# Kernel tuning notes

Measured on AMD Instinct MI355X. Metric: run time of the kernel, lower is better.

## Reference

```python
import jax, jax.numpy as jnp
import numpy as np


def _conv_nchw(x, w, strides):
    # F.conv2d with padding=0 -> VALID, NCHW / OIHW layout
    return jax.lax.conv_general_dilated(
        x, w, window_strides=tuple(strides), padding="VALID",
        dimension_numbers=("NCHW", "OIHW", "NCHW"))


def setup_inputs() -> dict:
    key = jax.random.key(0)
    kx, kw, kb = jax.random.split(key, 3)
    # scale so values span the full int8 range and all 8 bit-planes are active
    x = jax.random.normal(kx, (64, 64, 56, 56), dtype=jnp.float32) * 60.0
    weight = jax.random.normal(kw, (128, 64, 3, 3), dtype=jnp.float32) * 0.05
    bias = jax.random.normal(kb, (128,), dtype=jnp.float32)
    return {"x": x, "weight": weight, "bias": bias}


def reference(x, weight, bias):
    strides = (1, 1)
    # clamp to int8 range and cast (torch.clamp + .type(torch.int8))
    xi = jnp.clip(x, -128, 127).astype(jnp.int8)
    y = jnp.zeros((), dtype=weight.dtype)
    for i in range(8):
        # arithmetic shift on signed int8, matching torch semantics
        bit = ((xi >> i) & 1).astype(weight.dtype)
        yi = jnp.clip(_conv_nchw(bit, weight, strides), -1024, 1023)
        scale = jnp.asarray(-128.0 if i == 7 else float(2 ** i), dtype=weight.dtype)
        y = y + yi * scale
    y = y + bias.reshape(1, -1, 1, 1)
    return y
```

## Files before the change

### kernel.cpp

```cpp
#include <hip/hip_runtime.h>
#include <stdint.h>

typedef unsigned short u16;
typedef __attribute__((ext_vector_type(8))) __bf16 bf16x8;
typedef __attribute__((ext_vector_type(4))) float f32x4;

#define N_IMG 64
#define C_IN  64
#define HW_IN 3136
#define W_IN  56
#define C_OUT 128
#define OH    54
#define OW    54
#define SPI   2916
#define KTOT  576
#define M_TOTAL (N_IMG*SPI)

typedef __attribute__((address_space(3))) unsigned int lds_uint;
typedef __attribute__((address_space(1))) unsigned int gbl_uint;

__device__ __forceinline__ void load16_to_lds(const u16* g, u16* l) {
  __builtin_amdgcn_global_load_lds((const gbl_uint*)g, (lds_uint*)l, 16, 0, 0);
}

__device__ inline u16 f32_bf16_rne(float f) {
  unsigned u = __float_as_uint(f);
  u = (u + 0x7FFFu + ((u >> 16) & 1u)) >> 16;
  return (u16)u;
}

__global__ void convert_w(const float* __restrict__ w, u16* __restrict__ wtT) {
  int o = blockIdx.x * 256 + threadIdx.x;
  if (o >= C_OUT * KTOT) return;
  int co = o / KTOT;
  int k  = o - co * KTOT;
  int t  = k >> 6;
  int ci = k & 63;
  wtT[o] = f32_bf16_rne(w[co * KTOT + ci * 9 + t]);
}

__global__ __launch_bounds__(256) void convert_x(const float* __restrict__ x,
                                                 u16* __restrict__ xt) {
  __shared__ u16 tile[64][66];
  int n  = blockIdx.y;
  int s0 = blockIdx.x * 64;
  int tx = threadIdx.x, ty = threadIdx.y;
  const float* xp = x + (size_t)n * C_IN * HW_IN;
  #pragma unroll
  for (int i = ty; i < 64; i += 4) {
    float v = xp[i * HW_IN + s0 + tx];
    v = fminf(fmaxf(v, -128.f), 127.f);
    int iv = (int)v;
    tile[i][tx] = f32_bf16_rne((float)iv);
  }
  __syncthreads();
  u16* op = xt + (size_t)n * HW_IN * C_IN;
  #pragma unroll
  for (int i = ty; i < 64; i += 4) {
    op[(size_t)(s0 + i) * C_IN + tx] = tile[tx][i];
  }
}

__global__ __launch_bounds__(256) void conv_gemm(
    const u16* __restrict__ xt, const u16* __restrict__ wtT,
    const float* __restrict__ bias, float* __restrict__ y)
{
  __shared__ u16 sP[128 * 64];
  __shared__ u16 sW[128 * 64];

  int tid  = threadIdx.x;
  int wv   = tid >> 6;
  int lane = tid & 63;
  int ln   = lane & 15;
  int q    = lane >> 4;
  int wy   = wv >> 1;
  int wx   = wv & 1;

  int blk_sp0 = blockIdx.x * 128;

  int r8 = lane >> 3;
  int cg = lane & 7;
  int scol = (cg ^ r8) * 8;

  int pix_off[4], wt_off[4];
  #pragma unroll
  for (int j = 0; j < 4; j++) {
    int srow = wv * 32 + j * 8 + r8;
    int p   = blk_sp0 + srow;
    int img = p / SPI;  int rem = p - img * SPI;
    int oh  = rem / OW; int ow  = rem - oh * OW;
    pix_off[j] = (img * HW_IN + oh * W_IN + ow) * C_IN + scol;
    wt_off[j]  = srow * KTOT + scol;
  }

  f32x4 acc[4][4];
  #pragma unroll
  for (int mt = 0; mt < 4; mt++)
    #pragma unroll
    for (int nt = 0; nt < 4; nt++)
      acc[mt][nt] = (f32x4){0.f, 0.f, 0.f, 0.f};

  int wrow[4], prow[4];
  #pragma unroll
  for (int i = 0; i < 4; i++) {
    wrow[i] = (wy * 64 + i * 16 + ln) * 64;
    prow[i] = (wx * 64 + i * 16 + ln) * 64;
  }
  int l7 = ln & 7;

  #pragma unroll
  for (int kc = 0; kc < 9; kc++) {
    int kh = kc / 3, kw = kc - kh * 3;
    int xoff = (kh * W_IN + kw) * C_IN;

    __syncthreads();
    #pragma unroll
    for (int j = 0; j < 4; j++)
      load16_to_lds(xt + pix_off[j] + xoff, sP + (wv * 32 + j * 8) * 64);
    #pragma unroll
    for (int j = 0; j < 4; j++)
      load16_to_lds(wtT + wt_off[j] + kc * 64, sW + (wv * 32 + j * 8) * 64);
    __syncthreads();

    #pragma unroll
    for (int s = 0; s < 2; s++) {
      int pg = ((s * 4 + q) ^ l7) * 8;
      bf16x8 wf[4], pf[4];
      #pragma unroll
      for (int mt = 0; mt < 4; mt++)
        wf[mt] = *(const bf16x8*)(sW + wrow[mt] + pg);
      #pragma unroll
      for (int nt = 0; nt < 4; nt++)
        pf[nt] = *(const bf16x8*)(sP + prow[nt] + pg);
      #pragma unroll
      for (int mt = 0; mt < 4; mt++)
        #pragma unroll
        for (int nt = 0; nt < 4; nt++)
          acc[mt][nt] = __builtin_amdgcn_mfma_f32_16x16x32_bf16(
              wf[mt], pf[nt], acc[mt][nt], 0, 0, 0);
    }
  }

  #pragma unroll
  for (int nt = 0; nt < 4; nt++) {
    int p   = blk_sp0 + wx * 64 + nt * 16 + ln;
    int img = p / SPI;  int rem = p - img * SPI;
    int oh  = rem / OW; int ow  = rem - oh * OW;
    int obase = img * C_OUT * SPI + oh * OW + ow;
    #pragma unroll
    for (int mt = 0; mt < 4; mt++) {
      int co0 = wy * 64 + mt * 16 + q * 4;
      #pragma unroll
      for (int r = 0; r < 4; r++) {
        int co = co0 + r;
        y[obase + co * SPI] = acc[mt][nt][r] + bias[co];
      }
    }
  }
}

extern "C" void kernel_launch(void* const* d_in, const int* in_sizes, int n_in,
                              void* d_out, int out_size, void* d_ws, size_t ws_size,
                              hipStream_t stream) {
  const float* x    = (const float*)d_in[0];
  const float* w    = (const float*)d_in[1];
  const float* bias = (const float*)d_in[2];
  float* y = (float*)d_out;

  u16* wtT = (u16*)d_ws;
  u16* xt  = (u16*)((char*)d_ws + (size_t)C_OUT * KTOT * sizeof(u16));

  hipLaunchKernelGGL(convert_w, dim3((C_OUT * KTOT + 255) / 256), dim3(256), 0, stream,
                     w, wtT);
  hipLaunchKernelGGL(convert_x, dim3(HW_IN / 64, N_IMG), dim3(64, 4), 0, stream,
                     x, xt);
  hipLaunchKernelGGL(conv_gemm, dim3(M_TOTAL / 128), dim3(256), 0, stream,
                     xt, wtT, bias, y);
}
```

Baseline: 187.1 us.

## Double-buffer conv GEMM LDS tiles and fuse vectorized input/weight conversion

The conv GEMM now keeps two LDS buffers for the pixel and weight tiles. It prefetches the next 3x3 tap's slice while MFMAs run on the current one, which removes one barrier per tap and hides global-load latency. The separate weight and input conversion kernels are merged into one launch: an extra grid row handles the weights, and the input transpose uses 16-byte float4 loads and 8-wide u16 stores. The trade-off is that doubling LDS per block to 64 KB may lower how many blocks fit on each CU.

```diff
diff --git a/kernel.cpp b/kernel.cpp
--- a/kernel.cpp
+++ b/kernel.cpp
@@ -4,6 +4,8 @@
 typedef unsigned short u16;
 typedef __attribute__((ext_vector_type(8))) __bf16 bf16x8;
 typedef __attribute__((ext_vector_type(4))) float f32x4;
+typedef __attribute__((ext_vector_type(4))) u16 u16x4;
+typedef __attribute__((ext_vector_type(8))) u16 u16x8;
 
 #define N_IMG 64
 #define C_IN  64
@@ -29,35 +31,54 @@
   return (u16)u;
 }
 
-__global__ void convert_w(const float* __restrict__ w, u16* __restrict__ wtT) {
-  int o = blockIdx.x * 256 + threadIdx.x;
-  if (o >= C_OUT * KTOT) return;
-  int co = o / KTOT;
-  int k  = o - co * KTOT;
-  int t  = k >> 6;
-  int ci = k & 63;
-  wtT[o] = f32_bf16_rne(w[co * KTOT + ci * 9 + t]);
-}
-
-__global__ __launch_bounds__(256) void convert_x(const float* __restrict__ x,
-                                                 u16* __restrict__ xt) {
-  __shared__ u16 tile[64][66];
+__global__ __launch_bounds__(256) void convert_xw(
+    const float* __restrict__ x, const float* __restrict__ w,
+    u16* __restrict__ xt, u16* __restrict__ wtT)
+{
+  if (blockIdx.y == N_IMG) {
+    int o = blockIdx.x * 256 + threadIdx.x;
+    for (; o < C_OUT * KTOT; o += 49 * 256) {
+      int co = o / KTOT;
+      int k  = o - co * KTOT;
+      int t  = k >> 6;
+      int ci = k & 63;
+      wtT[o] = f32_bf16_rne(w[co * KTOT + ci * 9 + t]);
+    }
+    return;
+  }
+
+  __shared__ u16 tile[64][68];
   int n  = blockIdx.y;
   int s0 = blockIdx.x * 64;
-  int tx = threadIdx.x, ty = threadIdx.y;
-  const float* xp = x + (size_t)n * C_IN * HW_IN;
-  #pragma unroll
-  for (int i = ty; i < 64; i += 4) {
-    float v = xp[i * HW_IN + s0 + tx];
-    v = fminf(fmaxf(v, -128.f), 127.f);
-    int iv = (int)v;
-    tile[i][tx] = f32_bf16_rne((float)iv);
+  int t  = threadIdx.x;
+
+  int r = t >> 2;
+  int q = t & 3;
+  const float* xp = x + (size_t)n * C_IN * HW_IN + (size_t)r * HW_IN + s0 + q * 16;
+  #pragma unroll
+  for (int j = 0; j < 4; j++) {
+    f32x4 v = *(const f32x4*)(xp + 4 * j);
+    u16x4 o4;
+    #pragma unroll
+    for (int e = 0; e < 4; e++) {
+      float f = fminf(fmaxf(v[e], -128.f), 127.f);
+      int iv = (int)f;
+      o4[e] = f32_bf16_rne((float)iv);
+    }
+    *(u16x4*)&tile[r][q * 16 + 4 * j] = o4;
   }
   __syncthreads();
-  u16* op = xt + (size_t)n * HW_IN * C_IN;
-  #pragma unroll
-  for (int i = ty; i < 64; i += 4) {
-    op[(size_t)(s0 + i) * C_IN + tx] = tile[tx][i];
+
+  u16* op = xt + ((size_t)n * HW_IN + s0) * C_IN;
+  int g = t & 7;
+  int m = t >> 3;
+  #pragma unroll
+  for (int k2 = 0; k2 < 2; k2++) {
+    int sp = m * 2 + k2;
+    u16x8 o8;
+    #pragma unroll
+    for (int c = 0; c < 8; c++) o8[c] = tile[g * 8 + c][sp];
+    *(u16x8*)&op[(size_t)sp * C_IN + g * 8] = o8;
   }
 }
 
@@ -65,8 +86,8 @@
     const u16* __restrict__ xt, const u16* __restrict__ wtT,
     const float* __restrict__ bias, float* __restrict__ y)
 {
-  __shared__ u16 sP[128 * 64];
-  __shared__ u16 sW[128 * 64];
+  __shared__ u16 sP[2][128 * 64];
+  __shared__ u16 sW[2][128 * 64];
 
   int tid  = threadIdx.x;
   int wv   = tid >> 6;
@@ -107,20 +128,32 @@
     prow[i] = (wx * 64 + i * 16 + ln) * 64;
   }
   int l7 = ln & 7;
+  int lbase = (wv * 32) * 64;
+
+  #pragma unroll
+  for (int j = 0; j < 4; j++)
+    load16_to_lds(xt + pix_off[j], &sP[0][lbase + j * 8 * 64]);
+  #pragma unroll
+  for (int j = 0; j < 4; j++)
+    load16_to_lds(wtT + wt_off[j], &sW[0][lbase + j * 8 * 64]);
 
   #pragma unroll
   for (int kc = 0; kc < 9; kc++) {
-    int kh = kc / 3, kw = kc - kh * 3;
-    int xoff = (kh * W_IN + kw) * C_IN;
+    const int cur = kc & 1, nxt = cur ^ 1;
 
     __syncthreads();
-    #pragma unroll
-    for (int j = 0; j < 4; j++)
-      load16_to_lds(xt + pix_off[j] + xoff, sP + (wv * 32 + j * 8) * 64);
-    #pragma unroll
-    for (int j = 0; j < 4; j++)
-      load16_to_lds(wtT + wt_off[j] + kc * 64, sW + (wv * 32 + j * 8) * 64);
-    __syncthreads();
+
+    if (kc < 8) {
+      int kn = kc + 1;
+      int kh = kn / 3, kw = kn - kh * 3;
+      int xoff = (kh * W_IN + kw) * C_IN;
+      #pragma unroll
+      for (int j = 0; j < 4; j++)
+        load16_to_lds(xt + pix_off[j] + xoff, &sP[nxt][lbase + j * 8 * 64]);
+      #pragma unroll
+      for (int j = 0; j < 4; j++)
+        load16_to_lds(wtT + wt_off[j] + kn * 64, &sW[nxt][lbase + j * 8 * 64]);
+    }
 
     #pragma unroll
     for (int s = 0; s < 2; s++) {
@@ -128,10 +161,10 @@
       bf16x8 wf[4], pf[4];
       #pragma unroll
       for (int mt = 0; mt < 4; mt++)
-        wf[mt] = *(const bf16x8*)(sW + wrow[mt] + pg);
+        wf[mt] = *(const bf16x8*)(&sW[cur][0] + wrow[mt] + pg);
       #pragma unroll
       for (int nt = 0; nt < 4; nt++)
-        pf[nt] = *(const bf16x8*)(sP + prow[nt] + pg);
+        pf[nt] = *(const bf16x8*)(&sP[cur][0] + prow[nt] + pg);
       #pragma unroll
       for (int mt = 0; mt < 4; mt++)
         #pragma unroll
@@ -170,10 +203,8 @@
   u16* wtT = (u16*)d_ws;
   u16* xt  = (u16*)((char*)d_ws + (size_t)C_OUT * KTOT * sizeof(u16));
 
-  hipLaunchKernelGGL(convert_w, dim3((C_OUT * KTOT + 255) / 256), dim3(256), 0, stream,
-                     w, wtT);
-  hipLaunchKernelGGL(convert_x, dim3(HW_IN / 64, N_IMG), dim3(64, 4), 0, stream,
-                     x, xt);
+  hipLaunchKernelGGL(convert_xw, dim3(HW_IN / 64, N_IMG + 1), dim3(256), 0, stream,
+                     x, w, xt, wtT);
   hipLaunchKernelGGL(conv_gemm, dim3(M_TOTAL / 128), dim3(256), 0, stream,
                      xt, wtT, bias, y);
 }
```

Result: slower. 192.5 us (+2.9%).
